# Performance work log

Measured on AMD Instinct MI355X. Metric: run time of the kernel, lower is better.

## Reference

```python
import jax, jax.numpy as jnp
import numpy as np

B, C, H, W = 4, 512, 128, 128   # batch, in_channels, feature map HxW
KC = 256                        # key_channels
KP = 150                        # number of proxy regions (ADE20K classes)


def conv1x1(x, w, b):
    # x: [b,c,h,w], w: [k,c], b: [k] -> [b,k,h,w]
    return jnp.einsum('bchw,kc->bkhw', x, w) + b[None, :, None, None]


def proj2(x, w1, b1, w2, b2):
    # conv1x1-(BN folded)-relu twice, as in f_pixel / f_object
    h = jax.nn.relu(conv1x1(x, w1, b1))
    return jax.nn.relu(conv1x1(h, w2, b2))


def setup_inputs() -> dict:
    key = jax.random.key(0)
    ks = jax.random.split(key, 16)
    nrm = lambda k, shape, s=0.05: (jax.random.normal(k, shape, jnp.float32) * s)
    return {
        'x': jax.random.normal(ks[0], (B, C, H, W), jnp.float32),
        'proxy_feats': jax.random.normal(ks[1], (B, C, KP, 1), jnp.float32),
        # f_pixel: two 1x1 convs (BN in eval mode folded into weight+bias)
        'w_p1': nrm(ks[2], (KC, C)), 'b_p1': nrm(ks[3], (KC,)),
        'w_p2': nrm(ks[4], (KC, KC)), 'b_p2': nrm(ks[5], (KC,)),
        # f_object
        'w_o1': nrm(ks[6], (KC, C)), 'b_o1': nrm(ks[7], (KC,)),
        'w_o2': nrm(ks[8], (KC, KC)), 'b_o2': nrm(ks[9], (KC,)),
        # f_down
        'w_d': nrm(ks[10], (KC, C)), 'b_d': nrm(ks[11], (KC,)),
        # f_up
        'w_u': nrm(ks[12], (C, KC)), 'b_u': nrm(ks[13], (C,)),
    }


def reference(x, proxy_feats, w_p1, b_p1, w_p2, b_p2, w_o1, b_o1, w_o2, b_o2,
              w_d, b_d, w_u, b_u):
    b, _, h, w = x.shape
    n = h * w
    # query: [b, n, kc]
    query = proj2(x, w_p1, b_p1, w_p2, b_p2).reshape(b, KC, n).transpose(0, 2, 1)
    # key: [b, kc, kp]
    k = proj2(proxy_feats, w_o1, b_o1, w_o2, b_o2).reshape(b, KC, KP)
    # value: [b, kp, kc]
    v = jax.nn.relu(conv1x1(proxy_feats, w_d, b_d)).reshape(b, KC, KP).transpose(0, 2, 1)
    # scaled dot-product cross-attention
    sim = jnp.einsum('bnc,bck->bnk', query, k) * (KC ** -0.5)
    sim = jax.nn.softmax(sim, axis=-1)
    context = jnp.einsum('bnk,bkc->bnc', sim, v)            # [b, n, kc]
    context = context.transpose(0, 2, 1).reshape(b, KC, h, w)
    return jax.nn.relu(conv1x1(context, w_u, b_u))           # [b, C, h, w]
```

## Files before the change

kernel.cpp:

```cpp
#include <hip/hip_runtime.h>
#include <hip/hip_bf16.h>

#define NB   4
#define CIN  512
#define NPX  16384
#define KC   256
#define KP   150

#define LDH  264
#define LDP  200
#define LDX  72
#define SHSZ 16896
#define XBOF 7680

typedef __attribute__((ext_vector_type(8))) short short8;
typedef __attribute__((ext_vector_type(4))) float f32x4;
typedef __attribute__((ext_vector_type(4))) unsigned int u32x4;
typedef unsigned short u16;

__device__ __forceinline__ u16 f2bf(float f) {
    unsigned int u = __float_as_uint(f);
    return (u16)((u + 0x7FFFu + ((u >> 16) & 1u)) >> 16);
}
__device__ __forceinline__ unsigned cvtpk(float lo, float hi) {
    unsigned r;
    asm("v_cvt_pk_bf16_f32 %0, %1, %2" : "=v"(r) : "v"(lo), "v"(hi));
    return r;
}
__device__ __forceinline__ short8 ldfrag(const u16* __restrict__ p, int idx) {
    return *(const short8*)(p + ((long)idx << 3));
}

__global__ __launch_bounds__(256, 4)
void fused_kernel(const u16* __restrict__ wp1p, const float* __restrict__ xg,
                  const u16* __restrict__ wp2p, const float* __restrict__ bp1,
                  const float* __restrict__ bp2, const u16* __restrict__ keyp,
                  const u16* __restrict__ vp, const u16* __restrict__ wup,
                  const float* __restrict__ bu, float* __restrict__ outg)
{
    __shared__ u16 sh[SHSZ];

    const int b  = blockIdx.z;
    const int n0 = blockIdx.x * 64;
    const int tid = threadIdx.x, lane = tid & 63, wid = tid >> 6;
    const int rg = lane & 15, kg = lane >> 4;

    const float* xb = xg + (long)b * CIN * NPX;
    float* ob       = outg + (long)b * CIN * NPX;
    const u16* kyp  = keyp + (long)b * 40960;
    const u16* vbp  = vp   + (long)b * 40960;

    const int sxp = (tid & 31) * 2, sxg = tid >> 5;
    const float* xsrc = xb + (long)(sxg * 8) * NPX + n0 + sxp;
    u16* XB = sh + XBOF;

    float f0[8], f1[8];
    auto LOADX = [&](int kt) {
        #pragma unroll
        for (int e = 0; e < 8; ++e) {
            float2 v = *(const float2*)(xsrc + (long)(kt * 64 + e) * NPX);
            f0[e] = v.x; f1[e] = v.y;
        }
    };
    auto WRITEX = [&](int buf) {
        u32x4 w0, w1;
        w0.x = cvtpk(f0[0], f0[1]); w0.y = cvtpk(f0[2], f0[3]);
        w0.z = cvtpk(f0[4], f0[5]); w0.w = cvtpk(f0[6], f0[7]);
        w1.x = cvtpk(f1[0], f1[1]); w1.y = cvtpk(f1[2], f1[3]);
        w1.z = cvtpk(f1[4], f1[5]); w1.w = cvtpk(f1[6], f1[7]);
        *(u32x4*)(XB + buf * 4608 + sxp * LDX + sxg * 8) = w0;
        *(u32x4*)(XB + buf * 4608 + (sxp + 1) * LDX + sxg * 8) = w1;
    };

    f32x4 acc[4][4];
    #pragma unroll
    for (int i = 0; i < 4; ++i)
        #pragma unroll
        for (int j = 0; j < 4; ++j) acc[i][j] = (f32x4){0.f, 0.f, 0.f, 0.f};

    LOADX(0); WRITEX(0);
    __syncthreads();

    #pragma unroll 1
    for (int kt = 0; kt < 8; ++kt) {
        const int buf = kt & 1;
        if (kt < 7) LOADX(kt + 1);
        #pragma unroll 1
        for (int s = 0; s < 2; ++s) {
            short8 a[4];
            #pragma unroll
            for (int i = 0; i < 4; ++i)
                a[i] = ldfrag(wp1p, ((wid * 4 + i) * 16 + kt * 2 + s) * 64 + lane);
            __builtin_amdgcn_s_setprio(1);
            #pragma unroll
            for (int j = 0; j < 4; ++j) {
                short8 bb = *(const short8*)(XB + buf * 4608 + (j * 16 + rg) * LDX + (s * 4 + kg) * 8);
                #pragma unroll
                for (int i = 0; i < 4; ++i)
                    acc[i][j] = __builtin_amdgcn_mfma_f32_16x16x32_bf16(a[i], bb, acc[i][j], 0, 0, 0);
            }
            __builtin_amdgcn_s_setprio(0);
        }
        if (kt < 7) WRITEX(buf ^ 1);
        __syncthreads();
    }

    #pragma unroll
    for (int i = 0; i < 4; ++i) {
        const int kc4 = wid * 64 + i * 16 + kg * 4;
        const f32x4 bv = *(const f32x4*)(bp1 + kc4);
        #pragma unroll
        for (int j = 0; j < 4; ++j) {
            const int n = j * 16 + rg;
            uint2 pk;
            pk.x = cvtpk(fmaxf(acc[i][j][0] + bv.x, 0.f), fmaxf(acc[i][j][1] + bv.y, 0.f));
            pk.y = cvtpk(fmaxf(acc[i][j][2] + bv.z, 0.f), fmaxf(acc[i][j][3] + bv.w, 0.f));
            *(uint2*)(sh + n * LDH + kc4) = pk;
        }
    }
    __syncthreads();

    f32x4 acc2[4][4];
    #pragma unroll
    for (int i = 0; i < 4; ++i)
        #pragma unroll
        for (int j = 0; j < 4; ++j) acc2[i][j] = (f32x4){0.f, 0.f, 0.f, 0.f};

    #pragma unroll 1
    for (int S = 0; S < 8; ++S) {
        short8 a[4];
        #pragma unroll
        for (int i = 0; i < 4; ++i)
            a[i] = ldfrag(wp2p, ((wid * 4 + i) * 8 + S) * 64 + lane);
        __builtin_amdgcn_s_setprio(1);
        #pragma unroll
        for (int j = 0; j < 4; ++j) {
            short8 bb = *(const short8*)(sh + (j * 16 + rg) * LDH + S * 32 + kg * 8);
            #pragma unroll
            for (int i = 0; i < 4; ++i)
                acc2[i][j] = __builtin_amdgcn_mfma_f32_16x16x32_bf16(a[i], bb, acc2[i][j], 0, 0, 0);
        }
        __builtin_amdgcn_s_setprio(0);
    }
    __syncthreads();

    #pragma unroll
    for (int i = 0; i < 4; ++i) {
        const int kc4 = wid * 64 + i * 16 + kg * 4;
        const f32x4 bv = *(const f32x4*)(bp2 + kc4);
        #pragma unroll
        for (int j = 0; j < 4; ++j) {
            const int n = j * 16 + rg;
            uint2 pk;
            pk.x = cvtpk(fmaxf(acc2[i][j][0] + bv.x, 0.f), fmaxf(acc2[i][j][1] + bv.y, 0.f));
            pk.y = cvtpk(fmaxf(acc2[i][j][2] + bv.z, 0.f), fmaxf(acc2[i][j][3] + bv.w, 0.f));
            *(uint2*)(sh + n * LDH + kc4) = pk;
        }
    }
    __syncthreads();

    f32x4 s1[10];
    #pragma unroll
    for (int i = 0; i < 10; ++i) s1[i] = (f32x4){0.f, 0.f, 0.f, 0.f};
    #pragma unroll 1
    for (int s = 0; s < 8; ++s) {
        short8 bq = *(const short8*)(sh + (wid * 16 + rg) * LDH + s * 32 + kg * 8);
        __builtin_amdgcn_s_setprio(1);
        #pragma unroll
        for (int i = 0; i < 10; ++i) {
            short8 a = ldfrag(kyp, (i * 8 + s) * 64 + lane);
            s1[i] = __builtin_amdgcn_mfma_f32_16x16x32_bf16(a, bq, s1[i], 0, 0, 0);
        }
        __builtin_amdgcn_s_setprio(0);
    }
    float mx = -3.0e38f;
    #pragma unroll
    for (int i = 0; i < 9; ++i)
        #pragma unroll
        for (int r = 0; r < 4; ++r) mx = fmaxf(mx, s1[i][r]);
    #pragma unroll
    for (int r = 0; r < 4; ++r) if (kg * 4 + r < 6) mx = fmaxf(mx, s1[9][r]);
    mx = fmaxf(mx, __shfl_xor(mx, 16));
    mx = fmaxf(mx, __shfl_xor(mx, 32));
    float l = 0.f;
    #pragma unroll
    for (int i = 0; i < 10; ++i)
        #pragma unroll
        for (int r = 0; r < 4; ++r) {
            const bool valid = (i < 9) || (kg * 4 + r < 6);
            float e = valid ? __expf((s1[i][r] - mx) * 0.0625f) : 0.f;
            s1[i][r] = e; l += e;
        }
    l += __shfl_xor(l, 16);
    l += __shfl_xor(l, 32);
    const float inv = 1.f / l;
    __syncthreads();

    #pragma unroll
    for (int i = 0; i < 10; ++i) {
        uint2 pk;
        pk.x = cvtpk(s1[i][0] * inv, s1[i][1] * inv);
        pk.y = cvtpk(s1[i][2] * inv, s1[i][3] * inv);
        *(uint2*)(sh + (wid * 16 + rg) * LDP + i * 16 + kg * 4) = pk;
    }
    __syncthreads();

    f32x4 acc4[4][4];
    #pragma unroll
    for (int i = 0; i < 4; ++i)
        #pragma unroll
        for (int j = 0; j < 4; ++j) acc4[i][j] = (f32x4){0.f, 0.f, 0.f, 0.f};
    #pragma unroll 1
    for (int s = 0; s < 5; ++s) {
        short8 a[4];
        #pragma unroll
        for (int i = 0; i < 4; ++i)
            a[i] = ldfrag(vbp, ((wid * 4 + i) * 5 + s) * 64 + lane);
        __builtin_amdgcn_s_setprio(1);
        #pragma unroll
        for (int j = 0; j < 4; ++j) {
            short8 bb = *(const short8*)(sh + (j * 16 + rg) * LDP + s * 32 + kg * 8);
            #pragma unroll
            for (int i = 0; i < 4; ++i)
                acc4[i][j] = __builtin_amdgcn_mfma_f32_16x16x32_bf16(a[i], bb, acc4[i][j], 0, 0, 0);
        }
        __builtin_amdgcn_s_setprio(0);
    }
    __syncthreads();

    #pragma unroll
    for (int i = 0; i < 4; ++i) {
        const int kc4 = wid * 64 + i * 16 + kg * 4;
        #pragma unroll
        for (int j = 0; j < 4; ++j) {
            const int n = j * 16 + rg;
            uint2 pk;
            pk.x = cvtpk(acc4[i][j][0], acc4[i][j][1]);
            pk.y = cvtpk(acc4[i][j][2], acc4[i][j][3]);
            *(uint2*)(sh + n * LDH + kc4) = pk;
        }
    }
    __syncthreads();

    #pragma unroll 1
    for (int h2 = 0; h2 < 2; ++h2) {
        f32x4 a5[4][4];
        #pragma unroll
        for (int i = 0; i < 4; ++i)
            #pragma unroll
            for (int j = 0; j < 4; ++j) a5[i][j] = (f32x4){0.f, 0.f, 0.f, 0.f};
        #pragma unroll 1
        for (int S = 0; S < 8; ++S) {
            short8 a[4];
            #pragma unroll
            for (int i = 0; i < 4; ++i)
                a[i] = ldfrag(wup, ((h2 * 16 + wid * 4 + i) * 8 + S) * 64 + lane);
            __builtin_amdgcn_s_setprio(1);
            #pragma unroll
            for (int j = 0; j < 4; ++j) {
                short8 bb = *(const short8*)(sh + (j * 16 + rg) * LDH + S * 32 + kg * 8);
                #pragma unroll
                for (int i = 0; i < 4; ++i)
                    a5[i][j] = __builtin_amdgcn_mfma_f32_16x16x32_bf16(a[i], bb, a5[i][j], 0, 0, 0);
            }
            __builtin_amdgcn_s_setprio(0);
        }
        #pragma unroll
        for (int i = 0; i < 4; ++i) {
            const int c4 = h2 * 256 + wid * 64 + i * 16 + kg * 4;
            const f32x4 bv = *(const f32x4*)(bu + c4);
            #pragma unroll
            for (int j = 0; j < 4; ++j) {
                const int n = n0 + j * 16 + rg;
                ob[(long)(c4 + 0) * NPX + n] = fmaxf(a5[i][j][0] + bv.x, 0.f);
                ob[(long)(c4 + 1) * NPX + n] = fmaxf(a5[i][j][1] + bv.y, 0.f);
                ob[(long)(c4 + 2) * NPX + n] = fmaxf(a5[i][j][2] + bv.z, 0.f);
                ob[(long)(c4 + 3) * NPX + n] = fmaxf(a5[i][j][3] + bv.w, 0.f);
            }
        }
    }
}

__global__ __launch_bounds__(256)
void prep_kernel(const float* __restrict__ w_p1, const float* __restrict__ w_p2,
                 const float* __restrict__ w_u,  const float* __restrict__ w_o1,
                 const float* __restrict__ w_o2, const float* __restrict__ w_d,
                 u16* __restrict__ wp1p, u16* __restrict__ wp2p,
                 u16* __restrict__ wup, float* __restrict__ wo1T,
                 float* __restrict__ wdT, float* __restrict__ wo2T)
{
    const int i = blockIdx.x * 256 + threadIdx.x;
    const int j = i & 7, l = (i >> 3) & 63;
    {
        const int S = (i >> 9) & 15, R = i >> 13;
        wp1p[i] = f2bf(w_p1[(long)(R * 16 + (l & 15)) * CIN + S * 32 + ((l >> 4) << 3) + j]);
    }
    {
        const int S = (i >> 9) & 7, R = i >> 12;
        wup[i] = f2bf(w_u[(long)(R * 16 + (l & 15)) * KC + S * 32 + ((l >> 4) << 3) + j]);
    }
    {
        const int c = i >> 8, kc = i & 255;
        wo1T[i] = w_o1[(long)kc * CIN + c];
        wdT[i]  = w_d [(long)kc * CIN + c];
    }
    if (i < 65536) {
        const int S = (i >> 9) & 7, R = i >> 12;
        wp2p[i] = f2bf(w_p2[(long)(R * 16 + (l & 15)) * KC + S * 32 + ((l >> 4) << 3) + j]);
        const int c = i >> 8, kc = i & 255;
        wo2T[i] = w_o2[(long)kc * KC + c];
    }
}

__global__ __launch_bounds__(256)
void kv_kernel(const float* __restrict__ proxy,
               const float* __restrict__ wo1T, const float* __restrict__ b_o1,
               const float* __restrict__ wdT,  const float* __restrict__ b_d,
               const float* __restrict__ wo2T, const float* __restrict__ b_o2,
               u16* __restrict__ keyp, u16* __restrict__ vp)
{
    __shared__ float PX[CIN * 4];
    __shared__ float HL[4][KC];
    const int kp0 = blockIdx.x * 4;
    const int b   = blockIdx.y;
    const int kc  = threadIdx.x;

    #pragma unroll
    for (int it = 0; it < 8; ++it) {
        const int idx = it * 256 + kc;
        const int q = idx & 3, c = idx >> 2;
        const int kp = kp0 + q;
        PX[c * 4 + q] = (kp < KP) ? proxy[(long)b * CIN * KP + (long)c * KP + kp] : 0.f;
    }
    __syncthreads();

    float ah[4] = {0.f, 0.f, 0.f, 0.f}, av[4] = {0.f, 0.f, 0.f, 0.f};
    #pragma unroll 1
    for (int c0 = 0; c0 < CIN; c0 += 8) {
        float w1[8], wd[8];
        #pragma unroll
        for (int e = 0; e < 8; ++e) {
            w1[e] = wo1T[(long)(c0 + e) * KC + kc];
            wd[e] = wdT [(long)(c0 + e) * KC + kc];
        }
        #pragma unroll
        for (int e = 0; e < 8; ++e)
            #pragma unroll
            for (int q = 0; q < 4; ++q) {
                const float p = PX[(c0 + e) * 4 + q];
                ah[q] += w1[e] * p;
                av[q] += wd[e] * p;
            }
    }
    const float bo1 = b_o1[kc], bd = b_d[kc];
    #pragma unroll
    for (int q = 0; q < 4; ++q) {
        const int kp = kp0 + q;
        HL[q][kc] = fmaxf(ah[q] + bo1, 0.f);
        const float vv = (kp < KP) ? fmaxf(av[q] + bd, 0.f) : 0.f;
        const int idx2 = (((kc >> 4) * 5 + (kp >> 5)) * 64 +
                          ((kp >> 3) & 3) * 16 + (kc & 15)) * 8 + (kp & 7);
        vp[(long)b * 40960 + idx2] = f2bf(vv);
    }
    __syncthreads();

    float ak[4] = {0.f, 0.f, 0.f, 0.f};
    #pragma unroll 1
    for (int c0 = 0; c0 < KC; c0 += 8) {
        float w2[8];
        #pragma unroll
        for (int e = 0; e < 8; ++e)
            w2[e] = wo2T[(long)(c0 + e) * KC + kc];
        #pragma unroll
        for (int e = 0; e < 8; ++e)
            #pragma unroll
            for (int q = 0; q < 4; ++q)
                ak[q] += w2[e] * HL[q][c0 + e];
    }
    const float bo2 = b_o2[kc];
    #pragma unroll
    for (int q = 0; q < 4; ++q) {
        const int kp = kp0 + q;
        const float v = (kp < KP) ? fmaxf(ak[q] + bo2, 0.f) : 0.f;
        const int idx = (((kp >> 4) * 8 + (kc >> 5)) * 64 +
                         ((kc >> 3) & 3) * 16 + (kp & 15)) * 8 + (kc & 7);
        keyp[(long)b * 40960 + idx] = f2bf(v);
    }
}

extern "C" void kernel_launch(void* const* d_in, const int* in_sizes, int n_in,
                              void* d_out, int out_size, void* d_ws, size_t ws_size,
                              hipStream_t stream)
{
    const float* x     = (const float*)d_in[0];
    const float* proxy = (const float*)d_in[1];
    const float* w_p1  = (const float*)d_in[2];
    const float* b_p1  = (const float*)d_in[3];
    const float* w_p2  = (const float*)d_in[4];
    const float* b_p2  = (const float*)d_in[5];
    const float* w_o1  = (const float*)d_in[6];
    const float* b_o1  = (const float*)d_in[7];
    const float* w_o2  = (const float*)d_in[8];
    const float* b_o2  = (const float*)d_in[9];
    const float* w_d   = (const float*)d_in[10];
    const float* b_d   = (const float*)d_in[11];
    const float* w_u   = (const float*)d_in[12];
    const float* b_u   = (const float*)d_in[13];
    float* out = (float*)d_out;
    (void)in_sizes; (void)n_in; (void)out_size; (void)ws_size;

    char* ws = (char*)d_ws;
    size_t off = 0;
    auto alloc = [&](size_t bytes) { size_t o = off; off += (bytes + 255) & ~(size_t)255; return o; };

    u16*   wp1p = (u16*)  (ws + alloc((size_t)131072 * 2));
    u16*   wp2p = (u16*)  (ws + alloc((size_t)65536 * 2));
    u16*   wup  = (u16*)  (ws + alloc((size_t)131072 * 2));
    float* wo1T = (float*)(ws + alloc((size_t)131072 * 4));
    float* wdT  = (float*)(ws + alloc((size_t)131072 * 4));
    float* wo2T = (float*)(ws + alloc((size_t)65536 * 4));
    u16*   keyp = (u16*)  (ws + alloc((size_t)NB * 40960 * 2));
    u16*   vp   = (u16*)  (ws + alloc((size_t)NB * 40960 * 2));

    prep_kernel<<<512, 256, 0, stream>>>(
        w_p1, w_p2, w_u, w_o1, w_o2, w_d, wp1p, wp2p, wup, wo1T, wdT, wo2T);
    kv_kernel<<<dim3(40, NB), 256, 0, stream>>>(
        proxy, wo1T, b_o1, wdT, b_d, wo2T, b_o2, keyp, vp);
    fused_kernel<<<dim3(NPX / 64, 1, NB), 256, 0, stream>>>(
        wp1p, x, wp2p, b_p1, b_p2, keyp, vp, wup, b_u, out);
}
```

Measured before the change: 130.2 us.

## Widen x tile loads, deepen prefetch, and tile weight transposes in prep

Result: no change. 132.6 us (+1.8%).

```diff
diff --git a/kernel.cpp b/kernel.cpp
--- a/kernel.cpp
+++ b/kernel.cpp
@@ -50,26 +50,24 @@
     const u16* kyp  = keyp + (long)b * 40960;
     const u16* vbp  = vp   + (long)b * 40960;
 
-    const int sxp = (tid & 31) * 2, sxg = tid >> 5;
-    const float* xsrc = xb + (long)(sxg * 8) * NPX + n0 + sxp;
+    const int p0 = (tid & 15) * 4, c0g = tid >> 4;
+    const float* xsrc = xb + (long)(c0g * 4) * NPX + n0 + p0;
     u16* XB = sh + XBOF;
 
-    float f0[8], f1[8];
-    auto LOADX = [&](int kt) {
-        #pragma unroll
-        for (int e = 0; e < 8; ++e) {
-            float2 v = *(const float2*)(xsrc + (long)(kt * 64 + e) * NPX);
-            f0[e] = v.x; f1[e] = v.y;
-        }
+    f32x4 S0[4], S1[4];
+    auto LOADX = [&](f32x4 (&S)[4], int kt) {
+        #pragma unroll
+        for (int e = 0; e < 4; ++e)
+            S[e] = *(const f32x4*)(xsrc + (long)(kt * 64 + e) * NPX);
     };
-    auto WRITEX = [&](int buf) {
-        u32x4 w0, w1;
-        w0.x = cvtpk(f0[0], f0[1]); w0.y = cvtpk(f0[2], f0[3]);
-        w0.z = cvtpk(f0[4], f0[5]); w0.w = cvtpk(f0[6], f0[7]);
-        w1.x = cvtpk(f1[0], f1[1]); w1.y = cvtpk(f1[2], f1[3]);
-        w1.z = cvtpk(f1[4], f1[5]); w1.w = cvtpk(f1[6], f1[7]);
-        *(u32x4*)(XB + buf * 4608 + sxp * LDX + sxg * 8) = w0;
-        *(u32x4*)(XB + buf * 4608 + (sxp + 1) * LDX + sxg * 8) = w1;
+    auto WRITEX = [&](f32x4 (&S)[4], int buf) {
+        #pragma unroll
+        for (int j = 0; j < 4; ++j) {
+            uint2 pk;
+            pk.x = cvtpk(S[0][j], S[1][j]);
+            pk.y = cvtpk(S[2][j], S[3][j]);
+            *(uint2*)(XB + buf * 4608 + (p0 + j) * LDX + c0g * 4) = pk;
+        }
     };
 
     f32x4 acc[4][4];
@@ -78,13 +76,7 @@
         #pragma unroll
         for (int j = 0; j < 4; ++j) acc[i][j] = (f32x4){0.f, 0.f, 0.f, 0.f};
 
-    LOADX(0); WRITEX(0);
-    __syncthreads();
-
-    #pragma unroll 1
-    for (int kt = 0; kt < 8; ++kt) {
-        const int buf = kt & 1;
-        if (kt < 7) LOADX(kt + 1);
+    auto MFMA_G1 = [&](int buf, int kt) {
         #pragma unroll 1
         for (int s = 0; s < 2; ++s) {
             short8 a[4];
@@ -101,7 +93,21 @@
             }
             __builtin_amdgcn_s_setprio(0);
         }
-        if (kt < 7) WRITEX(buf ^ 1);
+    };
+
+    LOADX(S0, 0); WRITEX(S0, 0); LOADX(S0, 1);
+    __syncthreads();
+
+    #pragma unroll 1
+    for (int t4 = 0; t4 < 4; ++t4) {
+        const int ke = 2 * t4;
+        if (t4 < 3) LOADX(S1, ke + 2);
+        MFMA_G1(0, ke);
+        WRITEX(S0, 1);
+        __syncthreads();
+        if (t4 < 3) LOADX(S0, ke + 3);
+        MFMA_G1(1, ke + 1);
+        if (t4 < 3) WRITEX(S1, 0);
         __syncthreads();
     }
 
@@ -289,27 +295,40 @@
                  u16* __restrict__ wup, float* __restrict__ wo1T,
                  float* __restrict__ wdT, float* __restrict__ wo2T)
 {
-    const int i = blockIdx.x * 256 + threadIdx.x;
-    const int j = i & 7, l = (i >> 3) & 63;
-    {
-        const int S = (i >> 9) & 15, R = i >> 13;
-        wp1p[i] = f2bf(w_p1[(long)(R * 16 + (l & 15)) * CIN + S * 32 + ((l >> 4) << 3) + j]);
-    }
-    {
-        const int S = (i >> 9) & 7, R = i >> 12;
-        wup[i] = f2bf(w_u[(long)(R * 16 + (l & 15)) * KC + S * 32 + ((l >> 4) << 3) + j]);
-    }
-    {
-        const int c = i >> 8, kc = i & 255;
-        wo1T[i] = w_o1[(long)kc * CIN + c];
-        wdT[i]  = w_d [(long)kc * CIN + c];
-    }
-    if (i < 65536) {
-        const int S = (i >> 9) & 7, R = i >> 12;
-        wp2p[i] = f2bf(w_p2[(long)(R * 16 + (l & 15)) * KC + S * 32 + ((l >> 4) << 3) + j]);
-        const int c = i >> 8, kc = i & 255;
-        wo2T[i] = w_o2[(long)kc * KC + c];
-    }
+    const int bx = blockIdx.x;
+    const int tid = threadIdx.x;
+    if (bx < 512) {
+        const int i = bx * 256 + tid;
+        const int j = i & 7, l = (i >> 3) & 63;
+        {
+            const int S = (i >> 9) & 15, R = i >> 13;
+            wp1p[i] = f2bf(w_p1[(long)(R * 16 + (l & 15)) * CIN + S * 32 + ((l >> 4) << 3) + j]);
+        }
+        {
+            const int S = (i >> 9) & 7, R = i >> 12;
+            wup[i] = f2bf(w_u[(long)(R * 16 + (l & 15)) * KC + S * 32 + ((l >> 4) << 3) + j]);
+        }
+        if (i < 65536) {
+            const int S = (i >> 9) & 7, R = i >> 12;
+            wp2p[i] = f2bf(w_p2[(long)(R * 16 + (l & 15)) * KC + S * 32 + ((l >> 4) << 3) + j]);
+        }
+        return;
+    }
+    __shared__ float T[64][65];
+    int tb = bx - 512;
+    const float* src; float* dst; int srcC;
+    if (tb < 32)      { src = w_o1; dst = wo1T; srcC = CIN; }
+    else if (tb < 64) { tb -= 32; src = w_d; dst = wdT; srcC = CIN; }
+    else              { tb -= 64; src = w_o2; dst = wo2T; srcC = KC; }
+    const int r0 = (tb & 3) * 64, c0 = (tb >> 2) * 64;
+    const int lr = tid >> 6, lc = tid & 63;
+    #pragma unroll
+    for (int p = 0; p < 16; ++p)
+        T[p * 4 + lr][lc] = src[(long)(r0 + p * 4 + lr) * srcC + c0 + lc];
+    __syncthreads();
+    #pragma unroll
+    for (int p = 0; p < 16; ++p)
+        dst[(long)(c0 + p * 4 + lr) * KC + r0 + lc] = T[lc][p * 4 + lr];
 }
 
 __global__ __launch_bounds__(256)
@@ -422,7 +441,7 @@
     u16*   keyp = (u16*)  (ws + alloc((size_t)NB * 40960 * 2));
     u16*   vp   = (u16*)  (ws + alloc((size_t)NB * 40960 * 2));
 
-    prep_kernel<<<512, 256, 0, stream>>>(
+    prep_kernel<<<592, 256, 0, stream>>>(
         w_p1, w_p2, w_u, w_o1, w_o2, w_d, wp1p, wp2p, wup, wo1T, wdT, wo2T);
     kv_kernel<<<dim3(40, NB), 256, 0, stream>>>(
         proxy, wo1T, b_o1, wdT, b_d, wo2T, b_o2, keyp, vp);
```
